# Kernel tuning notes

Hardware: AMD Instinct MI355X
Metric: run time of the kernel (lower is better)

The kernel has to match this reference:

```python
import jax, jax.numpy as jnp
import numpy as np

D_MODEL = 2048
NUM_Q_HEADS = 16
NUM_KV_HEADS = 4
HEAD_DIM = D_MODEL // NUM_Q_HEADS  # 128
NUM_GROUPS = NUM_Q_HEADS // NUM_KV_HEADS  # 4
ROPE_BASE = 10000.0


def _rope_cos_sin(seq_len, head_dim):
    inv_freq = 1.0 / (ROPE_BASE ** (jnp.arange(0, head_dim, 2, dtype=jnp.float32) / head_dim))
    t = jnp.arange(seq_len, dtype=jnp.float32)
    freqs = jnp.outer(t, inv_freq)            # [S, head_dim/2]
    emb = jnp.concatenate([freqs, freqs], -1)  # [S, head_dim]
    return jnp.cos(emb)[None, :, None, :], jnp.sin(emb)[None, :, None, :]


def _rotate_half(x):
    half = x.shape[-1] // 2
    return jnp.concatenate([-x[..., half:], x[..., :half]], axis=-1)


def setup_inputs() -> dict:
    key = jax.random.key(0)
    k0, k1, k2, k3, k4 = jax.random.split(key, 5)
    B, S = 2, 2048
    kv_dim = HEAD_DIM * NUM_KV_HEADS
    scale = D_MODEL ** -0.5
    return {
        "x": jax.random.normal(k0, (B, S, D_MODEL), jnp.float32),
        "attention_mask": jnp.ones((B, S), jnp.int32),
        "Wq": jax.random.normal(k1, (D_MODEL, D_MODEL), jnp.float32) * scale,
        "Wk": jax.random.normal(k2, (D_MODEL, kv_dim), jnp.float32) * scale,
        "Wv": jax.random.normal(k3, (D_MODEL, kv_dim), jnp.float32) * scale,
        "Wo": jax.random.normal(k4, (D_MODEL, D_MODEL), jnp.float32) * scale,
    }


def reference(x, attention_mask, Wq, Wk, Wv, Wo):
    B, S, _ = x.shape
    q = (x @ Wq).reshape(B, S, NUM_Q_HEADS, HEAD_DIM)
    k = (x @ Wk).reshape(B, S, NUM_KV_HEADS, HEAD_DIM)
    v = (x @ Wv).reshape(B, S, NUM_KV_HEADS, HEAD_DIM)

    cos, sin = _rope_cos_sin(S, HEAD_DIM)  # [1,S,1,hd]
    q = q * cos + _rotate_half(q) * sin
    k = k * cos + _rotate_half(k) * sin

    # [B, H, S, hd]; replicate KV heads across groups (repeat_interleave)
    q = q.transpose(0, 2, 1, 3)
    k = jnp.repeat(k.transpose(0, 2, 1, 3), NUM_GROUPS, axis=1)
    v = jnp.repeat(v.transpose(0, 2, 1, 3), NUM_GROUPS, axis=1)

    scale = HEAD_DIM ** -0.5
    scores = jnp.einsum("bhqd,bhkd->bhqk", q, k) * scale
    mask = attention_mask[:, None, None, :]  # [B,1,1,S] over keys
    scores = jnp.where(mask == 0, jnp.float32(-jnp.inf), scores)
    probs = jax.nn.softmax(scores, axis=-1)
    out = jnp.einsum("bhqk,bhkd->bhqd", probs, v)
    out = out.transpose(0, 2, 1, 3).reshape(B, S, D_MODEL)
    return out @ Wo
```

## Files before the change

kernel.cpp:

```cpp
#include <hip/hip_runtime.h>
#include <hip/hip_bf16.h>

typedef __attribute__((ext_vector_type(4))) float f32x4;
typedef __attribute__((ext_vector_type(16))) float f32x16;
typedef __attribute__((ext_vector_type(8))) short s16x8;
typedef __attribute__((ext_vector_type(4))) short s16x4;
typedef __attribute__((ext_vector_type(2))) unsigned int u32x2;

__device__ __forceinline__ float fexp2(float x) {
    float y; asm("v_exp_f32 %0, %1" : "=v"(y) : "v"(x)); return y;
}

__global__ void rope_tables(float* __restrict__ cosT, float* __restrict__ sinT) {
    const int s = blockIdx.x, j = threadIdx.x;
    const double inv = pow(10000.0, -(double)j / 64.0);
    const double f = (double)s * inv;
    cosT[s * 64 + j] = (float)cos(f);
    sinT[s * 64 + j] = (float)sin(f);
}

__global__ void mask_bias(const int* __restrict__ mask, float* __restrict__ mb, int n) {
    const int i = blockIdx.x * 256 + threadIdx.x;
    if (i < n) mb[i] = (mask[i] == 0) ? -1e30f : 0.f;
}

__global__ __launch_bounds__(256)
void cast_f32_bf16(const float* __restrict__ src, __hip_bfloat16* __restrict__ dst, int n4) {
    const int i = blockIdx.x * 256 + threadIdx.x;
    if (i < n4) {
        f32x4 v = *reinterpret_cast<const f32x4*>(src + (size_t)i * 4);
        union { s16x4 v4; __hip_bfloat16 h[4]; } u;
#pragma unroll
        for (int j = 0; j < 4; ++j) u.h[j] = __float2bfloat16(v[j]);
        *reinterpret_cast<s16x4*>(dst + (size_t)i * 4) = u.v4;
    }
}

__global__ __launch_bounds__(256)
void transpose_cast(const float* __restrict__ src, __hip_bfloat16* __restrict__ dst,
                    int R, int C) {
    __shared__ __align__(16) float t[32][33];
    const int tx = threadIdx.x, ty = threadIdx.y;
    const int r0 = blockIdx.y * 32, c0 = blockIdx.x * 32;
#pragma unroll
    for (int i = 0; i < 32; i += 8)
        t[ty + i][tx] = src[(size_t)(r0 + ty + i) * C + c0 + tx];
    __syncthreads();
#pragma unroll
    for (int i = 0; i < 32; i += 8)
        dst[(size_t)(c0 + ty + i) * R + r0 + tx] = __float2bfloat16(t[tx][ty + i]);
}

__global__ __launch_bounds__(256)
void vt_transpose(const __hip_bfloat16* __restrict__ qkv, __hip_bfloat16* __restrict__ Vt) {
    __shared__ unsigned short t[32][33];
    const int tx = threadIdx.x, ty = threadIdx.y;
    const int s0 = blockIdx.x * 32, d0 = blockIdx.y * 32;
    const int bh = blockIdx.z, b = bh >> 2, hh = bh & 3;
    const unsigned short* q = (const unsigned short*)qkv;
#pragma unroll
    for (int i = 0; i < 32; i += 8)
        t[ty + i][tx] = q[(size_t)(b * 2048 + s0 + ty + i) * 3072 + 2560 + hh * 128 + d0 + tx];
    __syncthreads();
#pragma unroll
    for (int i = 0; i < 32; i += 8)
        ((unsigned short*)Vt)[((size_t)(bh * 128) + d0 + ty + i) * 2048 + s0 + tx] = t[tx][ty + i];
}

template<int NI, bool BF16OUT>
__global__ __launch_bounds__(512, 1)
void gemm256_bt(const __hip_bfloat16* __restrict__ A,
                const __hip_bfloat16* __restrict__ Bt,
                void* __restrict__ Cv, int M, int N, int K, int NX) {
    constexpr int NB = NI / 2;
    __shared__ __align__(16) __hip_bfloat16 sm[4][2][8192];
    const int tid = threadIdx.x;
    const int l = tid & 63, w = tid >> 6;
    const int lo = l & 15, hi = l >> 4;
    const int wm = w >> 2, wn = w & 3;
    const int id = blockIdx.x, slot = id >> 3;
    const int by = (id & 7) * 2 + slot / NX;
    const int bx = slot % NX;
    const int row0 = by * 256;
    const int col0 = bx * (NI * 64);
    const int nk = K >> 5;

    f32x4 acc[8][NI];
#pragma unroll
    for (int mi = 0; mi < 8; ++mi)
#pragma unroll
        for (int ni = 0; ni < NI; ++ni) acc[mi][ni] = f32x4{0.f, 0.f, 0.f, 0.f};

    auto stage = [&](int kt) {
        const int s = kt & 3, k0 = kt << 5;
#pragma unroll
        for (int i = 0; i < 2; ++i) {
            const int c = i * 512 + tid;
            const int r = c >> 2, sw = ((c & 3) ^ ((r >> 1) & 3)) * 8;
            __builtin_amdgcn_global_load_lds(
                (const __attribute__((address_space(1))) void*)(A + (size_t)(row0 + r) * K + k0 + sw),
                (__attribute__((address_space(3))) void*)(&sm[s][0][c * 8]), 16, 0, 0);
        }
#pragma unroll
        for (int i = 0; i < NB; ++i) {
            const int c = i * 512 + tid;
            const int r = c >> 2, sw = ((c & 3) ^ ((r >> 1) & 3)) * 8;
            __builtin_amdgcn_global_load_lds(
                (const __attribute__((address_space(1))) void*)(Bt + (size_t)(col0 + r) * K + k0 + sw),
                (__attribute__((address_space(3))) void*)(&sm[s][1][c * 8]), 16, 0, 0);
        }
    };

    stage(0); stage(1); stage(2);
    for (int kt = 0; kt < nk; ++kt) {
        const int s = kt & 3;
        if (kt < nk - 2) {
            if constexpr (NI == 4) asm volatile("s_waitcnt vmcnt(8)" ::: "memory");
            else                   asm volatile("s_waitcnt vmcnt(6)" ::: "memory");
        } else if (kt == nk - 2) {
            if constexpr (NI == 4) asm volatile("s_waitcnt vmcnt(4)" ::: "memory");
            else                   asm volatile("s_waitcnt vmcnt(3)" ::: "memory");
        } else {
            asm volatile("s_waitcnt vmcnt(0)" ::: "memory");
        }
        asm volatile("s_waitcnt lgkmcnt(0)" ::: "memory");
        asm volatile("s_barrier" ::: "memory");
        if (kt + 3 < nk) stage(kt + 3);

        s16x8 af[8], bf[NI];
        const int rsw = ((lo >> 1) & 3);
#pragma unroll
        for (int mi = 0; mi < 8; ++mi)
            af[mi] = *reinterpret_cast<const s16x8*>(
                &sm[s][0][(wm * 128 + mi * 16 + lo) * 32 + ((hi ^ rsw) * 8)]);
#pragma unroll
        for (int ni = 0; ni < NI; ++ni)
            bf[ni] = *reinterpret_cast<const s16x8*>(
                &sm[s][1][(wn * NI * 16 + ni * 16 + lo) * 32 + ((hi ^ rsw) * 8)]);
        __builtin_amdgcn_s_setprio(1);
#pragma unroll
        for (int mi = 0; mi < 8; ++mi)
#pragma unroll
            for (int ni = 0; ni < NI; ++ni)
                acc[mi][ni] = __builtin_amdgcn_mfma_f32_16x16x32_bf16(af[mi], bf[ni], acc[mi][ni], 0, 0, 0);
        __builtin_amdgcn_s_setprio(0);
    }
    const int rbase = row0 + wm * 128 + hi * 4;
    const int cbase = col0 + wn * NI * 16 + lo;
    if constexpr (BF16OUT) {
        __hip_bfloat16* C = (__hip_bfloat16*)Cv;
#pragma unroll
        for (int mi = 0; mi < 8; ++mi)
#pragma unroll
            for (int ni = 0; ni < NI; ++ni)
#pragma unroll
                for (int r = 0; r < 4; ++r)
                    C[(size_t)(rbase + mi * 16 + r) * N + cbase + ni * 16] =
                        __float2bfloat16(acc[mi][ni][r]);
    } else {
        float* C = (float*)Cv;
#pragma unroll
        for (int mi = 0; mi < 8; ++mi)
#pragma unroll
            for (int ni = 0; ni < NI; ++ni)
#pragma unroll
                for (int r = 0; r < 4; ++r)
                    C[(size_t)(rbase + mi * 16 + r) * N + cbase + ni * 16] = acc[mi][ni][r];
    }
}

__global__ __launch_bounds__(256)
void rope_scatter(const __hip_bfloat16* __restrict__ qkv,
                  const float* __restrict__ cosT, const float* __restrict__ sinT,
                  __hip_bfloat16* __restrict__ Qr, __hip_bfloat16* __restrict__ Kr) {
    const int m = blockIdx.y;
    const int col4 = blockIdx.x * 256 + threadIdx.x;
    if (col4 >= 640) return;
    const int col = col4 * 4;
    const int b = m >> 11, s = m & 2047;
    const int d = col & 127;
    const int j = d & 63;
    union { s16x4 v4; __hip_bfloat16 h[4]; } vv, pp, u;
    vv.v4 = *reinterpret_cast<const s16x4*>(qkv + (size_t)m * 3072 + col);
    pp.v4 = *reinterpret_cast<const s16x4*>(qkv + (size_t)m * 3072 + (col ^ 64));
    const f32x4 c4 = *reinterpret_cast<const f32x4*>(cosT + s * 64 + j);
    const f32x4 s4 = *reinterpret_cast<const f32x4*>(sinT + s * 64 + j);
    const float sgn = (d < 64) ? -1.f : 1.f;
#pragma unroll
    for (int i = 0; i < 4; ++i)
        u.h[i] = __float2bfloat16(__bfloat162float(vv.h[i]) * c4[i] +
                                  sgn * __bfloat162float(pp.h[i]) * s4[i]);
    if (col < 2048) {
        const int hh = col >> 7;
        *reinterpret_cast<s16x4*>(&Qr[((size_t)(b * 16 + hh) * 2048 + s) * 128 + d]) = u.v4;
    } else {
        const int hh = (col - 2048) >> 7;
        *reinterpret_cast<s16x4*>(&Kr[((size_t)(b * 4 + hh) * 2048 + s) * 128 + d]) = u.v4;
    }
}

__global__ __launch_bounds__(256, 2)
void attn_kernel(const __hip_bfloat16* __restrict__ Qr,
                 const __hip_bfloat16* __restrict__ Kr,
                 const __hip_bfloat16* __restrict__ Vt,
                 const float* __restrict__ maskb,
                 __hip_bfloat16* __restrict__ Oo) {
    const int S = 2048;
    const int qt = blockIdx.x;
    const int bh = blockIdx.y;
    const int b = bh >> 4, h = bh & 15, kvh = h >> 2;
    const int tid = threadIdx.x;
    const int l = tid & 63, wv_ = tid >> 6;
    const int lq = l & 31, hi2 = l >> 5;
    __shared__ __align__(16) __hip_bfloat16 Ks[2][64 * 128];
    __shared__ __align__(16) __hip_bfloat16 Vs[2][128 * 64];

    const __hip_bfloat16* Qb = Qr + (size_t)(b * 16 + h) * S * 128;
    const __hip_bfloat16* Kb = Kr + (size_t)(b * 4 + kvh) * S * 128;
    const __hip_bfloat16* Vb = Vt + (size_t)(b * 4 + kvh) * 128 * S;
    const float* mrow = maskb + b * S;

    const int qrow = qt * 128 + wv_ * 32 + lq;
    s16x8 qf[8];
#pragma unroll
    for (int ks = 0; ks < 8; ++ks)
        qf[ks] = *reinterpret_cast<const s16x8*>(Qb + (size_t)qrow * 128 + ks * 16 + hi2 * 8);

    float m_run = 0.f, l_run = 0.f;
    f32x16 o[4];
#pragma unroll
    for (int dt = 0; dt < 4; ++dt)
#pragma unroll
        for (int r = 0; r < 16; ++r) o[dt][r] = 0.f;
    const float scale2 = 0.12751682f;

    const int krow = tid >> 4, kc8 = tid & 15;
    const int koff = (kc8 ^ (krow & 7)) * 8;
    const int vrow = tid >> 3, vc8 = tid & 7;
    const int voff = (vc8 ^ (vrow & 7)) * 8;

    s16x8 kreg[4], vreg[4];
    auto load_tile = [&](int kv0) {
#pragma unroll
        for (int i = 0; i < 4; ++i)
            kreg[i] = *reinterpret_cast<const s16x8*>(
                Kb + (size_t)(kv0 + i * 16 + krow) * 128 + kc8 * 8);
#pragma unroll
        for (int i = 0; i < 4; ++i)
            vreg[i] = *reinterpret_cast<const s16x8*>(
                Vb + (size_t)(i * 32 + vrow) * S + kv0 + vc8 * 8);
    };

    auto body = [&](int kt, __hip_bfloat16* Kc, __hip_bfloat16* Vc) {
        const int kv0 = kt * 64;
        f32x4 bi[2][4];
#pragma unroll
        for (int sub = 0; sub < 2; ++sub)
#pragma unroll
            for (int r4 = 0; r4 < 4; ++r4)
                bi[sub][r4] = *reinterpret_cast<const f32x4*>(
                    mrow + kv0 + sub * 32 + r4 * 8 + hi2 * 4);
#pragma unroll
        for (int i = 0; i < 4; ++i)
            *reinterpret_cast<s16x8*>(Kc + (i * 16 + krow) * 128 + koff) = kreg[i];
#pragma unroll
        for (int i = 0; i < 4; ++i)
            *reinterpret_cast<s16x8*>(Vc + (i * 32 + vrow) * 64 + voff) = vreg[i];
        if (kt < 31) load_tile(kv0 + 64);
        asm volatile("s_waitcnt lgkmcnt(0)" ::: "memory");
        asm volatile("s_barrier" ::: "memory");

        f32x16 sc[2];
#pragma unroll
        for (int sub = 0; sub < 2; ++sub)
#pragma unroll
            for (int r = 0; r < 16; ++r) sc[sub][r] = 0.f;
        __builtin_amdgcn_s_setprio(1);
#pragma unroll
        for (int sub = 0; sub < 2; ++sub) {
            const int kr = sub * 32 + lq;
            const int ksw = kr & 7;
#pragma unroll
            for (int ks = 0; ks < 8; ++ks) {
                s16x8 kf = *reinterpret_cast<const s16x8*>(
                    Kc + kr * 128 + (((ks * 2 + hi2) ^ ksw) * 8));
                sc[sub] = __builtin_amdgcn_mfma_f32_32x32x16_bf16(kf, qf[ks], sc[sub], 0, 0, 0);
            }
        }
        __builtin_amdgcn_s_setprio(0);
#pragma unroll
        for (int sub = 0; sub < 2; ++sub)
#pragma unroll
            for (int r = 0; r < 16; ++r)
                sc[sub][r] = fmaf(sc[sub][r], scale2, bi[sub][r >> 2][r & 3]);
        float mx = sc[0][0];
#pragma unroll
        for (int sub = 0; sub < 2; ++sub)
#pragma unroll
            for (int r = 0; r < 16; ++r) mx = fmaxf(mx, sc[sub][r]);
        float ss = 0.f;
#pragma unroll
        for (int sub = 0; sub < 2; ++sub)
#pragma unroll
            for (int r = 0; r < 16; ++r) {
                sc[sub][r] = fexp2(sc[sub][r] - m_run);
                ss += sc[sub][r];
            }
        mx = fmaxf(mx, __shfl_xor(mx, 32));
        if (__ballot(mx > m_run + 11.5417f) != 0ull) {
            const float mnew = fmaxf(m_run, mx);
            const float alpha = fexp2(m_run - mnew);
            m_run = mnew;
            l_run *= alpha;
            ss *= alpha;
#pragma unroll
            for (int sub = 0; sub < 2; ++sub)
#pragma unroll
                for (int r = 0; r < 16; ++r) sc[sub][r] *= alpha;
#pragma unroll
            for (int dt = 0; dt < 4; ++dt)
#pragma unroll
                for (int r = 0; r < 16; ++r) o[dt][r] *= alpha;
        }
        ss += __shfl_xor(ss, 32);
        l_run += ss;
        unsigned int wvp[8][2];
#pragma unroll
        for (int g = 0; g < 8; ++g) {
            const int sub = g >> 2, r4 = g & 3;
            asm("v_cvt_pk_bf16_f32 %0, %1, %2"
                : "=v"(wvp[g][0]) : "v"(sc[sub][r4 * 4 + 0]), "v"(sc[sub][r4 * 4 + 1]));
            asm("v_cvt_pk_bf16_f32 %0, %1, %2"
                : "=v"(wvp[g][1]) : "v"(sc[sub][r4 * 4 + 2]), "v"(sc[sub][r4 * 4 + 3]));
        }
        __builtin_amdgcn_s_setprio(1);
#pragma unroll
        for (int ks = 0; ks < 4; ++ks) {
            u32x2 r0 = __builtin_amdgcn_permlane32_swap(wvp[2 * ks][0], wvp[2 * ks + 1][0], false, false);
            u32x2 r1 = __builtin_amdgcn_permlane32_swap(wvp[2 * ks][1], wvp[2 * ks + 1][1], false, false);
            union { unsigned int u[4]; s16x8 v; } pf;
            pf.u[0] = r0.x; pf.u[1] = r1.x; pf.u[2] = r0.y; pf.u[3] = r1.y;
#pragma unroll
            for (int dt = 0; dt < 4; ++dt) {
                const int dvr = dt * 32 + lq;
                s16x8 vf = *reinterpret_cast<const s16x8*>(
                    Vc + dvr * 64 + (((ks * 2 + hi2) ^ (dvr & 7)) * 8));
                o[dt] = __builtin_amdgcn_mfma_f32_32x32x16_bf16(vf, pf.v, o[dt], 0, 0, 0);
            }
        }
        __builtin_amdgcn_s_setprio(0);
    };

    load_tile(0);
    for (int kt2 = 0; kt2 < 16; ++kt2) {
        body(2 * kt2,     &Ks[0][0], &Vs[0][0]);
        body(2 * kt2 + 1, &Ks[1][0], &Vs[1][0]);
    }
    const float inv = 1.f / l_run;
    const size_t obase = (size_t)(b * S + qt * 128 + wv_ * 32 + lq) * 2048 + h * 128;
#pragma unroll
    for (int dt = 0; dt < 4; ++dt)
#pragma unroll
        for (int r4 = 0; r4 < 4; ++r4) {
            union { s16x4 v4; __hip_bfloat16 hh[4]; } u;
#pragma unroll
            for (int j = 0; j < 4; ++j)
                u.hh[j] = __float2bfloat16(o[dt][r4 * 4 + j] * inv);
            *reinterpret_cast<s16x4*>(&Oo[obase + dt * 32 + r4 * 8 + hi2 * 4]) = u.v4;
        }
}

extern "C" void kernel_launch(void* const* d_in, const int* in_sizes, int n_in,
                              void* d_out, int out_size, void* d_ws, size_t ws_size,
                              hipStream_t stream) {
    const float* x  = (const float*)d_in[0];
    const int* mask = (const int*)d_in[1];
    const float* Wq = (const float*)d_in[2];
    const float* Wk = (const float*)d_in[3];
    const float* Wv = (const float*)d_in[4];
    const float* Wo = (const float*)d_in[5];
    float* out = (float*)d_out;

    char* ws = (char*)d_ws;
    size_t off = 0;
    auto alloc = [&](size_t bytes) -> void* {
        void* p = ws + off;
        off += (bytes + 255) & ~(size_t)255;
        return p;
    };
    __hip_bfloat16* xb     = (__hip_bfloat16*)alloc(4096ULL * 2048 * 2);
    __hip_bfloat16* wqkv_t = (__hip_bfloat16*)alloc(3072ULL * 2048 * 2);
    __hip_bfloat16* wo_t   = (__hip_bfloat16*)alloc(2048ULL * 2048 * 2);
    __hip_bfloat16* qkvb   = (__hip_bfloat16*)alloc(4096ULL * 3072 * 2);
    __hip_bfloat16* Kr     = (__hip_bfloat16*)alloc(2ULL * 4 * 2048 * 128 * 2);
    __hip_bfloat16* Vt     = (__hip_bfloat16*)alloc(2ULL * 4 * 2048 * 128 * 2);
    float*          cosT   = (float*)alloc(2048ULL * 64 * 4);
    float*          sinT   = (float*)alloc(2048ULL * 64 * 4);
    float*          maskb  = (float*)alloc(2ULL * 2048 * 4);
    __hip_bfloat16* attno  = (__hip_bfloat16*)alloc(4096ULL * 2048 * 2);
    __hip_bfloat16* Qr    = xb;

    rope_tables<<<dim3(2048), dim3(64), 0, stream>>>(cosT, sinT);
    mask_bias<<<dim3(16), dim3(256), 0, stream>>>(mask, maskb, 4096);
    cast_f32_bf16<<<dim3(8192), dim3(256), 0, stream>>>(x, xb, 2097152);
    transpose_cast<<<dim3(64, 64), dim3(32, 8), 0, stream>>>(Wq, wqkv_t, 2048, 2048);
    transpose_cast<<<dim3(16, 64), dim3(32, 8), 0, stream>>>(Wk, wqkv_t + 2048ULL * 2048, 2048, 512);
    transpose_cast<<<dim3(16, 64), dim3(32, 8), 0, stream>>>(Wv, wqkv_t + 2560ULL * 2048, 2048, 512);
    transpose_cast<<<dim3(64, 64), dim3(32, 8), 0, stream>>>(Wo, wo_t, 2048, 2048);

    gemm256_bt<4, true><<<dim3(192), dim3(512), 0, stream>>>(xb, wqkv_t, qkvb, 4096, 3072, 2048, 12);
    rope_scatter<<<dim3(3, 4096), dim3(256), 0, stream>>>(qkvb, cosT, sinT, Qr, Kr);
    vt_transpose<<<dim3(64, 4, 8), dim3(32, 8), 0, stream>>>(qkvb, Vt);
    attn_kernel<<<dim3(16, 32), dim3(256), 0, stream>>>(Qr, Kr, Vt, maskb, attno);
    gemm256_bt<2, false><<<dim3(256), dim3(512), 0, stream>>>(attno, wo_t, out, 4096, 2048, 2048, 16);
}
```

Baseline: 226.0 us.

## Restructure attention with direct global-to-LDS loads, smaller tiles, and fused weight transposes

The attention kernel now runs 128-thread blocks over 64 query rows and 32-key tiles. K/V tiles are staged with global_load_lds straight into swizzled shared memory, replacing the register round trip, and the 1D grid is remapped to spread heads across CUs. The four weight transpose launches are merged into one kernel, and the RoPE table now uses single-precision math instead of double. Smaller tiles mean more barriers per key and less reuse of each K/V tile, traded for higher occupancy and fewer register-to-LDS stores.

```diff
diff --git a/kernel.cpp b/kernel.cpp
--- a/kernel.cpp
+++ b/kernel.cpp
@@ -13,10 +13,10 @@
 
 __global__ void rope_tables(float* __restrict__ cosT, float* __restrict__ sinT) {
     const int s = blockIdx.x, j = threadIdx.x;
-    const double inv = pow(10000.0, -(double)j / 64.0);
-    const double f = (double)s * inv;
-    cosT[s * 64 + j] = (float)cos(f);
-    sinT[s * 64 + j] = (float)sin(f);
+    const float inv = exp2f(-(float)j * (13.287712379549449f / 64.f));
+    const float f = (float)s * inv;
+    cosT[s * 64 + j] = cosf(f);
+    sinT[s * 64 + j] = sinf(f);
 }
 
 __global__ void mask_bias(const int* __restrict__ mask, float* __restrict__ mb, int n) {
@@ -37,18 +37,25 @@
 }
 
 __global__ __launch_bounds__(256)
-void transpose_cast(const float* __restrict__ src, __hip_bfloat16* __restrict__ dst,
-                    int R, int C) {
+void transpose_cast_all(const float* __restrict__ Wq, const float* __restrict__ Wk,
+                        const float* __restrict__ Wv, const float* __restrict__ Wo,
+                        __hip_bfloat16* __restrict__ wqkv_t, __hip_bfloat16* __restrict__ wo_t) {
     __shared__ __align__(16) float t[32][33];
     const int tx = threadIdx.x, ty = threadIdx.y;
-    const int r0 = blockIdx.y * 32, c0 = blockIdx.x * 32;
+    const int xseg = blockIdx.x;
+    const int r0 = blockIdx.y * 32;
+    const float* src; __hip_bfloat16* dst; int C, c0;
+    if (xseg < 64)      { src = Wq; dst = wqkv_t;                  C = 2048; c0 = xseg * 32; }
+    else if (xseg < 80) { src = Wk; dst = wqkv_t + 2048ULL * 2048; C = 512;  c0 = (xseg - 64) * 32; }
+    else if (xseg < 96) { src = Wv; dst = wqkv_t + 2560ULL * 2048; C = 512;  c0 = (xseg - 80) * 32; }
+    else                { src = Wo; dst = wo_t;                    C = 2048; c0 = (xseg - 96) * 32; }
 #pragma unroll
     for (int i = 0; i < 32; i += 8)
         t[ty + i][tx] = src[(size_t)(r0 + ty + i) * C + c0 + tx];
     __syncthreads();
 #pragma unroll
     for (int i = 0; i < 32; i += 8)
-        dst[(size_t)(c0 + ty + i) * R + r0 + tx] = __float2bfloat16(t[tx][ty + i]);
+        dst[(size_t)(c0 + ty + i) * 2048 + r0 + tx] = __float2bfloat16(t[tx][ty + i]);
 }
 
 __global__ __launch_bounds__(256)
@@ -199,28 +206,30 @@
     }
 }
 
-__global__ __launch_bounds__(256, 2)
+__global__ __launch_bounds__(128, 3)
 void attn_kernel(const __hip_bfloat16* __restrict__ Qr,
                  const __hip_bfloat16* __restrict__ Kr,
                  const __hip_bfloat16* __restrict__ Vt,
                  const float* __restrict__ maskb,
                  __hip_bfloat16* __restrict__ Oo) {
     const int S = 2048;
-    const int qt = blockIdx.x;
-    const int bh = blockIdx.y;
+    const int id = blockIdx.x;
+    const int v = (id & 7) * 128 + (id >> 3);
+    const int qt = v & 31;
+    const int bh = v >> 5;
     const int b = bh >> 4, h = bh & 15, kvh = h >> 2;
     const int tid = threadIdx.x;
-    const int l = tid & 63, wv_ = tid >> 6;
+    const int l = tid & 63, w = tid >> 6;
     const int lq = l & 31, hi2 = l >> 5;
-    __shared__ __align__(16) __hip_bfloat16 Ks[2][64 * 128];
-    __shared__ __align__(16) __hip_bfloat16 Vs[2][128 * 64];
+    __shared__ __align__(16) __hip_bfloat16 Ks[2][32 * 128];
+    __shared__ __align__(16) __hip_bfloat16 Vs[2][128 * 32];
 
     const __hip_bfloat16* Qb = Qr + (size_t)(b * 16 + h) * S * 128;
     const __hip_bfloat16* Kb = Kr + (size_t)(b * 4 + kvh) * S * 128;
     const __hip_bfloat16* Vb = Vt + (size_t)(b * 4 + kvh) * 128 * S;
     const float* mrow = maskb + b * S;
 
-    const int qrow = qt * 128 + wv_ * 32 + lq;
+    const int qrow = qt * 64 + w * 32 + lq;
     s16x8 qf[8];
 #pragma unroll
     for (int ks = 0; ks < 8; ++ks)
@@ -234,78 +243,56 @@
         for (int r = 0; r < 16; ++r) o[dt][r] = 0.f;
     const float scale2 = 0.12751682f;
 
-    const int krow = tid >> 4, kc8 = tid & 15;
-    const int koff = (kc8 ^ (krow & 7)) * 8;
-    const int vrow = tid >> 3, vc8 = tid & 7;
-    const int voff = (vc8 ^ (vrow & 7)) * 8;
-
-    s16x8 kreg[4], vreg[4];
-    auto load_tile = [&](int kv0) {
-#pragma unroll
-        for (int i = 0; i < 4; ++i)
-            kreg[i] = *reinterpret_cast<const s16x8*>(
-                Kb + (size_t)(kv0 + i * 16 + krow) * 128 + kc8 * 8);
-#pragma unroll
-        for (int i = 0; i < 4; ++i)
-            vreg[i] = *reinterpret_cast<const s16x8*>(
-                Vb + (size_t)(i * 32 + vrow) * S + kv0 + vc8 * 8);
+    auto stage = [&](int kt) {
+        const int buf = kt & 1;
+        const __hip_bfloat16* Kbt = Kb + (size_t)(kt * 32) * 128;
+        const __hip_bfloat16* Vbt = Vb + kt * 32;
+#pragma unroll
+        for (int i = 0; i < 4; ++i) {
+            const int c = (w * 4 + i) * 64 + l;
+            const int row = c >> 4, p = c & 15;
+            __builtin_amdgcn_global_load_lds(
+                (const __attribute__((address_space(1))) void*)(Kbt + row * 128 + ((p ^ (row & 7)) * 8)),
+                (__attribute__((address_space(3))) void*)(&Ks[buf][(w * 4 + i) * 512]), 16, 0, 0);
+        }
+#pragma unroll
+        for (int i = 0; i < 4; ++i) {
+            const int c = (w * 4 + i) * 64 + l;
+            const int row = c >> 2, p = c & 3;
+            __builtin_amdgcn_global_load_lds(
+                (const __attribute__((address_space(1))) void*)(Vbt + (size_t)row * S + (((p - (row >> 1)) & 3) * 8)),
+                (__attribute__((address_space(3))) void*)(&Vs[buf][(w * 4 + i) * 512]), 16, 0, 0);
+        }
     };
 
-    auto body = [&](int kt, __hip_bfloat16* Kc, __hip_bfloat16* Vc) {
-        const int kv0 = kt * 64;
-        f32x4 bi[2][4];
-#pragma unroll
-        for (int sub = 0; sub < 2; ++sub)
-#pragma unroll
-            for (int r4 = 0; r4 < 4; ++r4)
-                bi[sub][r4] = *reinterpret_cast<const f32x4*>(
-                    mrow + kv0 + sub * 32 + r4 * 8 + hi2 * 4);
-#pragma unroll
-        for (int i = 0; i < 4; ++i)
-            *reinterpret_cast<s16x8*>(Kc + (i * 16 + krow) * 128 + koff) = kreg[i];
-#pragma unroll
-        for (int i = 0; i < 4; ++i)
-            *reinterpret_cast<s16x8*>(Vc + (i * 32 + vrow) * 64 + voff) = vreg[i];
-        if (kt < 31) load_tile(kv0 + 64);
-        asm volatile("s_waitcnt lgkmcnt(0)" ::: "memory");
-        asm volatile("s_barrier" ::: "memory");
-
-        f32x16 sc[2];
-#pragma unroll
-        for (int sub = 0; sub < 2; ++sub)
-#pragma unroll
-            for (int r = 0; r < 16; ++r) sc[sub][r] = 0.f;
+    auto body = [&](const f32x4* bi, const __hip_bfloat16* Kc, const __hip_bfloat16* Vc) {
+        f32x16 sA, sB;
+#pragma unroll
+        for (int r = 0; r < 16; ++r) { sA[r] = 0.f; sB[r] = 0.f; }
         __builtin_amdgcn_s_setprio(1);
 #pragma unroll
-        for (int sub = 0; sub < 2; ++sub) {
-            const int kr = sub * 32 + lq;
-            const int ksw = kr & 7;
-#pragma unroll
-            for (int ks = 0; ks < 8; ++ks) {
-                s16x8 kf = *reinterpret_cast<const s16x8*>(
-                    Kc + kr * 128 + (((ks * 2 + hi2) ^ ksw) * 8));
-                sc[sub] = __builtin_amdgcn_mfma_f32_32x32x16_bf16(kf, qf[ks], sc[sub], 0, 0, 0);
-            }
+        for (int ks = 0; ks < 4; ++ks) {
+            s16x8 kf = *reinterpret_cast<const s16x8*>(
+                Kc + lq * 128 + (((ks * 2 + hi2) ^ (lq & 7)) * 8));
+            sA = __builtin_amdgcn_mfma_f32_32x32x16_bf16(kf, qf[ks], sA, 0, 0, 0);
+        }
+#pragma unroll
+        for (int ks = 4; ks < 8; ++ks) {
+            s16x8 kf = *reinterpret_cast<const s16x8*>(
+                Kc + lq * 128 + (((ks * 2 + hi2) ^ (lq & 7)) * 8));
+            sB = __builtin_amdgcn_mfma_f32_32x32x16_bf16(kf, qf[ks], sB, 0, 0, 0);
         }
         __builtin_amdgcn_s_setprio(0);
-#pragma unroll
-        for (int sub = 0; sub < 2; ++sub)
-#pragma unroll
-            for (int r = 0; r < 16; ++r)
-                sc[sub][r] = fmaf(sc[sub][r], scale2, bi[sub][r >> 2][r & 3]);
-        float mx = sc[0][0];
-#pragma unroll
-        for (int sub = 0; sub < 2; ++sub)
-#pragma unroll
-            for (int r = 0; r < 16; ++r) mx = fmaxf(mx, sc[sub][r]);
+        f32x16 sc;
+#pragma unroll
+        for (int r = 0; r < 16; ++r)
+            sc[r] = fmaf(sA[r] + sB[r], scale2, bi[r >> 2][r & 3]);
+        float mx = sc[0];
+#pragma unroll
+        for (int r = 1; r < 16; ++r) mx = fmaxf(mx, sc[r]);
         float ss = 0.f;
 #pragma unroll
-        for (int sub = 0; sub < 2; ++sub)
-#pragma unroll
-            for (int r = 0; r < 16; ++r) {
-                sc[sub][r] = fexp2(sc[sub][r] - m_run);
-                ss += sc[sub][r];
-            }
+        for (int r = 0; r < 16; ++r) { sc[r] = fexp2(sc[r] - m_run); ss += sc[r]; }
         mx = fmaxf(mx, __shfl_xor(mx, 32));
         if (__ballot(mx > m_run + 11.5417f) != 0ull) {
             const float mnew = fmaxf(m_run, mx);
@@ -314,9 +301,7 @@
             l_run *= alpha;
             ss *= alpha;
 #pragma unroll
-            for (int sub = 0; sub < 2; ++sub)
-#pragma unroll
-                for (int r = 0; r < 16; ++r) sc[sub][r] *= alpha;
+            for (int r = 0; r < 16; ++r) sc[r] *= alpha;
 #pragma unroll
             for (int dt = 0; dt < 4; ++dt)
 #pragma unroll
@@ -324,18 +309,17 @@
         }
         ss += __shfl_xor(ss, 32);
         l_run += ss;
-        unsigned int wvp[8][2];
-#pragma unroll
-        for (int g = 0; g < 8; ++g) {
-            const int sub = g >> 2, r4 = g & 3;
+        unsigned int wvp[4][2];
+#pragma unroll
+        for (int g = 0; g < 4; ++g) {
             asm("v_cvt_pk_bf16_f32 %0, %1, %2"
-                : "=v"(wvp[g][0]) : "v"(sc[sub][r4 * 4 + 0]), "v"(sc[sub][r4 * 4 + 1]));
+                : "=v"(wvp[g][0]) : "v"(sc[g * 4 + 0]), "v"(sc[g * 4 + 1]));
             asm("v_cvt_pk_bf16_f32 %0, %1, %2"
-                : "=v"(wvp[g][1]) : "v"(sc[sub][r4 * 4 + 2]), "v"(sc[sub][r4 * 4 + 3]));
+                : "=v"(wvp[g][1]) : "v"(sc[g * 4 + 2]), "v"(sc[g * 4 + 3]));
         }
         __builtin_amdgcn_s_setprio(1);
 #pragma unroll
-        for (int ks = 0; ks < 4; ++ks) {
+        for (int ks = 0; ks < 2; ++ks) {
             u32x2 r0 = __builtin_amdgcn_permlane32_swap(wvp[2 * ks][0], wvp[2 * ks + 1][0], false, false);
             u32x2 r1 = __builtin_amdgcn_permlane32_swap(wvp[2 * ks][1], wvp[2 * ks + 1][1], false, false);
             union { unsigned int u[4]; s16x8 v; } pf;
@@ -344,20 +328,36 @@
             for (int dt = 0; dt < 4; ++dt) {
                 const int dvr = dt * 32 + lq;
                 s16x8 vf = *reinterpret_cast<const s16x8*>(
-                    Vc + dvr * 64 + (((ks * 2 + hi2) ^ (dvr & 7)) * 8));
+                    Vc + dvr * 32 + ((((ks * 2 + hi2) + (dvr >> 1)) & 3) * 8));
                 o[dt] = __builtin_amdgcn_mfma_f32_32x32x16_bf16(vf, pf.v, o[dt], 0, 0, 0);
             }
         }
         __builtin_amdgcn_s_setprio(0);
     };
 
-    load_tile(0);
-    for (int kt2 = 0; kt2 < 16; ++kt2) {
-        body(2 * kt2,     &Ks[0][0], &Vs[0][0]);
-        body(2 * kt2 + 1, &Ks[1][0], &Vs[1][0]);
+    stage(0);
+    for (int t2 = 0; t2 < 32; ++t2) {
+        asm volatile("s_waitcnt vmcnt(0)" ::: "memory");
+        asm volatile("s_barrier" ::: "memory");
+        f32x4 biA[4];
+#pragma unroll
+        for (int r4 = 0; r4 < 4; ++r4)
+            biA[r4] = *reinterpret_cast<const f32x4*>(
+                mrow + t2 * 64 + r4 * 8 + hi2 * 4);
+        stage(2 * t2 + 1);
+        body(biA, &Ks[0][0], &Vs[0][0]);
+        asm volatile("s_waitcnt vmcnt(0)" ::: "memory");
+        asm volatile("s_barrier" ::: "memory");
+        f32x4 biB[4];
+#pragma unroll
+        for (int r4 = 0; r4 < 4; ++r4)
+            biB[r4] = *reinterpret_cast<const f32x4*>(
+                mrow + t2 * 64 + 32 + r4 * 8 + hi2 * 4);
+        if (t2 < 31) stage(2 * t2 + 2);
+        body(biB, &Ks[1][0], &Vs[1][0]);
     }
     const float inv = 1.f / l_run;
-    const size_t obase = (size_t)(b * S + qt * 128 + wv_ * 32 + lq) * 2048 + h * 128;
+    const size_t obase = (size_t)(b * S + qt * 64 + w * 32 + lq) * 2048 + h * 128;
 #pragma unroll
     for (int dt = 0; dt < 4; ++dt)
 #pragma unroll
@@ -403,14 +403,11 @@
     rope_tables<<<dim3(2048), dim3(64), 0, stream>>>(cosT, sinT);
     mask_bias<<<dim3(16), dim3(256), 0, stream>>>(mask, maskb, 4096);
     cast_f32_bf16<<<dim3(8192), dim3(256), 0, stream>>>(x, xb, 2097152);
-    transpose_cast<<<dim3(64, 64), dim3(32, 8), 0, stream>>>(Wq, wqkv_t, 2048, 2048);
-    transpose_cast<<<dim3(16, 64), dim3(32, 8), 0, stream>>>(Wk, wqkv_t + 2048ULL * 2048, 2048, 512);
-    transpose_cast<<<dim3(16, 64), dim3(32, 8), 0, stream>>>(Wv, wqkv_t + 2560ULL * 2048, 2048, 512);
-    transpose_cast<<<dim3(64, 64), dim3(32, 8), 0, stream>>>(Wo, wo_t, 2048, 2048);
+    transpose_cast_all<<<dim3(160, 64), dim3(32, 8), 0, stream>>>(Wq, Wk, Wv, Wo, wqkv_t, wo_t);
 
     gemm256_bt<4, true><<<dim3(192), dim3(512), 0, stream>>>(xb, wqkv_t, qkvb, 4096, 3072, 2048, 12);
     rope_scatter<<<dim3(3, 4096), dim3(256), 0, stream>>>(qkvb, cosT, sinT, Qr, Kr);
     vt_transpose<<<dim3(64, 4, 8), dim3(32, 8), 0, stream>>>(qkvb, Vt);
-    attn_kernel<<<dim3(16, 32), dim3(256), 0, stream>>>(Qr, Kr, Vt, maskb, attno);
+    attn_kernel<<<dim3(1024), dim3(128), 0, stream>>>(Qr, Kr, Vt, maskb, attno);
     gemm256_bt<2, false><<<dim3(256), dim3(512), 0, stream>>>(attno, wo_t, out, 4096, 2048, 2048, 16);
 }
```

After: 334.8 us. +48.1%, slower.
